# Kernel tuning notes

Hardware: AMD Instinct MI355X
Metric: run time of the kernel (lower is better)

The kernel has to match this reference:

```python
import jax, jax.numpy as jnp
import numpy as np

FEATURE_DIM = 512
NUM_HEADS = 8
HEAD_DIM = FEATURE_DIM // NUM_HEADS
B, L = 4, 2048


def setup_inputs() -> dict:
    key = jax.random.key(0)
    ks = jax.random.split(key, 10)
    s = 1.0 / np.sqrt(FEATURE_DIM)
    inp = {
        "ppg": jax.random.normal(ks[0], (B, FEATURE_DIM, L), dtype=jnp.float32),
        "ecg": jax.random.normal(ks[1], (B, FEATURE_DIM, L), dtype=jnp.float32),
        "Wq": jax.random.uniform(ks[2], (FEATURE_DIM, FEATURE_DIM), jnp.float32, -s, s),
        "bq": jnp.zeros((FEATURE_DIM,), jnp.float32),
        "Wk": jax.random.uniform(ks[3], (FEATURE_DIM, FEATURE_DIM), jnp.float32, -s, s),
        "bk": jnp.zeros((FEATURE_DIM,), jnp.float32),
        "Wv": jax.random.uniform(ks[4], (FEATURE_DIM, FEATURE_DIM), jnp.float32, -s, s),
        "bv": jnp.zeros((FEATURE_DIM,), jnp.float32),
        "Wo": jax.random.uniform(ks[5], (FEATURE_DIM, FEATURE_DIM), jnp.float32, -s, s),
        "bo": jnp.zeros((FEATURE_DIM,), jnp.float32),
    }
    return inp


def reference(ppg, ecg, Wq, bq, Wk, bk, Wv, bv, Wo, bo):
    # ppg/ecg: (B, C, L) -> (B, L, C)
    x = jnp.transpose(ppg, (0, 2, 1))
    y = jnp.transpose(ecg, (0, 2, 1))
    q = x @ Wq.T + bq  # (B, L, C)
    k = y @ Wk.T + bk
    v = y @ Wv.T + bv
    # split heads: (B, H, L, D)
    def split(t):
        return jnp.transpose(t.reshape(B, L, NUM_HEADS, HEAD_DIM), (0, 2, 1, 3))
    qh, kh, vh = split(q), split(k), split(v)
    scores = jnp.einsum('bhqd,bhkd->bhqk', qh, kh) / jnp.sqrt(jnp.float32(HEAD_DIM))
    probs = jax.nn.softmax(scores, axis=-1)  # dropout is identity in eval mode
    ctx = jnp.einsum('bhqk,bhkd->bhqd', probs, vh)
    ctx = jnp.transpose(ctx, (0, 2, 1, 3)).reshape(B, L, FEATURE_DIM)
    out = ctx @ Wo.T + bo + x  # residual with transposed ppg
    return jnp.transpose(out, (0, 2, 1))  # (B, C, L)
```

## Files before the change

### kernel.cpp

```cpp
#include <hip/hip_runtime.h>
#include <hip/hip_bf16.h>

static constexpr int Bc = 4;
static constexpr int Lc = 2048;
static constexpr int Cc = 512;
static constexpr int Hc = 8;
static constexpr int Dc = 64;

using short8  = __attribute__((ext_vector_type(8))) short;
using float4v = __attribute__((ext_vector_type(4))) float;

static __device__ __forceinline__ unsigned short f2bf(float f) {
    __hip_bfloat16 h = __float2bfloat16(f);
    return *reinterpret_cast<unsigned short*>(&h);
}
static __device__ __forceinline__ float bf2f(unsigned short u) {
    return __uint_as_float(((unsigned int)u) << 16);
}

__global__ __launch_bounds__(256) void prep_kernel(
    const float* __restrict__ ppg, const float* __restrict__ ecg,
    const float* __restrict__ Wq, const float* __restrict__ Wk,
    const float* __restrict__ Wv, const float* __restrict__ Wo,
    unsigned short* __restrict__ Xt_ppg, unsigned short* __restrict__ Xt_ecg,
    unsigned short* __restrict__ Wbf)
{
    __shared__ float Ts[64 * 69];
    const int task = blockIdx.x;
    const int tid  = threadIdx.x;

    if (task < 2048) {
        const int src = task >> 10;
        const int rem = task & 1023;
        const int b   = rem >> 8;
        const int c0  = ((rem >> 5) & 7) * 64;
        const int l0  = (rem & 31) * 64;
        const float* X = src ? ecg : ppg;
        unsigned short* Xt = src ? Xt_ecg : Xt_ppg;

        #pragma unroll
        for (int j = 0; j < 4; ++j) {
            int idx = tid + j * 256;
            int c = idx >> 4, l4 = idx & 15;
            float4 v = *(const float4*)(X + ((size_t)b * Cc + c0 + c) * Lc + l0 + l4 * 4);
            Ts[c * 69 + l4 * 4 + 0] = v.x;
            Ts[c * 69 + l4 * 4 + 1] = v.y;
            Ts[c * 69 + l4 * 4 + 2] = v.z;
            Ts[c * 69 + l4 * 4 + 3] = v.w;
        }
        __syncthreads();
        #pragma unroll
        for (int j = 0; j < 8; ++j) {
            int u = tid + j * 256;
            int l = u >> 5, p2 = u & 31;
            float a = Ts[(2 * p2) * 69 + l];
            float bb = Ts[(2 * p2 + 1) * 69 + l];
            ushort2 pk; pk.x = f2bf(a); pk.y = f2bf(bb);
            *(ushort2*)(Xt + ((size_t)b * Lc + l0 + l) * Cc + c0 + 2 * p2) = pk;
        }
    } else {
        const int wb   = task - 2048;
        const int widx = wb >> 7;
        const float* W = widx == 0 ? Wq : widx == 1 ? Wk : widx == 2 ? Wv : Wo;
        size_t off = (size_t)(wb & 127) * 2048 + (size_t)tid * 8;
        float4 v0 = *(const float4*)(W + off);
        float4 v1 = *(const float4*)(W + off + 4);
        unsigned short pk[8] = {f2bf(v0.x), f2bf(v0.y), f2bf(v0.z), f2bf(v0.w),
                                f2bf(v1.x), f2bf(v1.y), f2bf(v1.z), f2bf(v1.w)};
        *(short8*)(Wbf + (size_t)widx * Cc * Cc + off) = *(const short8*)pk;
    }
}

__global__ __launch_bounds__(256) void proj_kernel(
    const unsigned short* __restrict__ Xt_ppg,
    const unsigned short* __restrict__ Xt_ecg,
    const unsigned short* __restrict__ Wbf,
    const float* __restrict__ bq, const float* __restrict__ bk,
    const float* __restrict__ bv,
    unsigned short* __restrict__ Qw, unsigned short* __restrict__ Kw,
    unsigned short* __restrict__ Vtw)
{
    constexpr int LDW = 72;
    const int z = blockIdx.z, p = z >> 2, b = z & 3;
    const int l0 = blockIdx.x * 128, n0 = blockIdx.y * 128;
    const unsigned short* X = (p == 0) ? Xt_ppg : Xt_ecg;
    const unsigned short* W = Wbf + (size_t)p * Cc * Cc;
    const float* bias = (p == 0) ? bq : (p == 1) ? bk : bv;

    const int tid = threadIdx.x, wave = tid >> 6, lane = tid & 63;
    const int l16 = lane & 15, quad = lane >> 4;
    const int wr = wave >> 1, wc = wave & 1;

    __shared__ __align__(16) unsigned short At[128 * LDW];
    __shared__ __align__(16) unsigned short Bt[128 * LDW];

    float4v acc[4][4] = {};
    short8 areg[4], breg[4];

    const int srow = tid >> 3, sc8 = tid & 7;
    #pragma unroll
    for (int j = 0; j < 4; ++j) {
        areg[j] = *(const short8*)(X + ((size_t)b * Lc + l0 + srow + j * 32) * Cc + sc8 * 8);
        breg[j] = *(const short8*)(W + (size_t)(n0 + srow + j * 32) * Cc + sc8 * 8);
    }

    for (int c0 = 0; c0 < Cc; c0 += 64) {
        #pragma unroll
        for (int j = 0; j < 4; ++j) {
            *(short8*)&At[(srow + j * 32) * LDW + sc8 * 8] = areg[j];
            *(short8*)&Bt[(srow + j * 32) * LDW + sc8 * 8] = breg[j];
        }
        __syncthreads();

        if (c0 + 64 < Cc) {
            #pragma unroll
            for (int j = 0; j < 4; ++j) {
                areg[j] = *(const short8*)(X + ((size_t)b * Lc + l0 + srow + j * 32) * Cc
                                           + c0 + 64 + sc8 * 8);
                breg[j] = *(const short8*)(W + (size_t)(n0 + srow + j * 32) * Cc
                                           + c0 + 64 + sc8 * 8);
            }
        }

        const unsigned short* Am = (p < 2) ? At : Bt;
        const unsigned short* Bm = (p < 2) ? Bt : At;

        #pragma unroll
        for (int ks = 0; ks < 2; ++ks) {
            short8 bf[4];
            #pragma unroll
            for (int nt = 0; nt < 4; ++nt)
                bf[nt] = *(const short8*)&Bm[(wc * 64 + nt * 16 + l16) * LDW
                                             + ks * 32 + quad * 8];
            #pragma unroll
            for (int mt = 0; mt < 4; ++mt) {
                short8 af = *(const short8*)&Am[(wr * 64 + mt * 16 + l16) * LDW
                                                + ks * 32 + quad * 8];
                #pragma unroll
                for (int nt = 0; nt < 4; ++nt)
                    acc[mt][nt] = __builtin_amdgcn_mfma_f32_16x16x32_bf16(
                        af, bf[nt], acc[mt][nt], 0, 0, 0);
            }
        }
        __syncthreads();
    }

    if (p < 2) {
        const float sc = (p == 0) ? 0.18033688011112042f : 1.0f;
        unsigned short* dst = (p == 0) ? Qw : Kw;
        #pragma unroll
        for (int nt = 0; nt < 4; ++nt) {
            int n = n0 + wc * 64 + nt * 16 + l16;
            int h = n >> 6, d = n & 63;
            int bh = b * Hc + h;
            float bia = bias[n];
            #pragma unroll
            for (int mt = 0; mt < 4; ++mt) {
                #pragma unroll
                for (int r = 0; r < 4; ++r) {
                    int l = l0 + wr * 64 + mt * 16 + quad * 4 + r;
                    dst[((size_t)bh * Lc + l) * Dc + d] =
                        f2bf((acc[mt][nt][r] + bia) * sc);
                }
            }
        }
    } else {
        #pragma unroll
        for (int mt = 0; mt < 4; ++mt) {
            #pragma unroll
            for (int r = 0; r < 4; ++r) {
                int n = n0 + wr * 64 + mt * 16 + quad * 4 + r;
                int h = n >> 6, d = n & 63;
                int bh = b * Hc + h;
                float bia = bias[n];
                #pragma unroll
                for (int nt = 0; nt < 4; ++nt) {
                    int l = l0 + wc * 64 + nt * 16 + l16;
                    Vtw[((size_t)bh * Dc + d) * Lc + l] = f2bf(acc[mt][nt][r] + bia);
                }
            }
        }
    }
}

__global__ __launch_bounds__(256, 4) void attn_mfma_kernel(
    const unsigned short* __restrict__ Qg,
    const unsigned short* __restrict__ Kg,
    const unsigned short* __restrict__ Vtg,
    unsigned short* __restrict__ O0,
    unsigned short* __restrict__ O1,
    float* __restrict__ lpart)
{
    constexpr int LDW = 72;
    const int bh    = blockIdx.y;
    const int split = blockIdx.z;
    const int q0    = blockIdx.x * 128;
    const int tid   = threadIdx.x;
    const int wave  = tid >> 6;
    const int lane  = tid & 63;
    const int l16   = lane & 15;
    const int quad  = lane >> 4;

    __shared__ __align__(16) unsigned short Kt[64 * LDW];
    __shared__ __align__(16) unsigned short Vt[64 * LDW];
    __shared__ __align__(16) unsigned short PT[128 * LDW];

    const int srow = tid >> 3, sc8 = tid & 7;

    const unsigned short* Qb = Qg + ((size_t)bh * Lc + q0) * Dc;
    #pragma unroll
    for (int j = 0; j < 4; ++j)
        *(short8*)&PT[(srow + j * 32) * LDW + sc8 * 8] =
            *(const short8*)(Qb + (srow + j * 32) * Dc + sc8 * 8);
    __syncthreads();

    short8 qf[2][2];
    #pragma unroll
    for (int qt = 0; qt < 2; ++qt)
        #pragma unroll
        for (int ks = 0; ks < 2; ++ks)
            qf[qt][ks] = *(const short8*)&PT[(wave * 32 + qt * 16 + l16) * LDW
                                             + ks * 32 + quad * 8];

    float4v O[2][4] = {};
    float lsum[2] = {0.0f, 0.0f};

    const unsigned short* Kb0 = Kg + (size_t)bh * Lc * Dc;
    const unsigned short* Vb0 = Vtg + (size_t)bh * (Dc * Lc);
    const int kbase = split * (Lc / 2);

    short8 kreg[2], vreg[2];
    #pragma unroll
    for (int j = 0; j < 2; ++j) {
        kreg[j] = *(const short8*)(Kb0 + (size_t)(kbase + srow + j * 32) * Dc + sc8 * 8);
        vreg[j] = *(const short8*)(Vb0 + (size_t)(srow + j * 32) * Lc + kbase + sc8 * 8);
    }

    for (int kc = kbase; kc < kbase + Lc / 2; kc += 64) {
        #pragma unroll
        for (int j = 0; j < 2; ++j) {
            *(short8*)&Kt[(srow + j * 32) * LDW + sc8 * 8] = kreg[j];
            *(short8*)&Vt[(srow + j * 32) * LDW + sc8 * 8] = vreg[j];
        }
        __syncthreads();

        if (kc + 64 < kbase + Lc / 2) {
            #pragma unroll
            for (int j = 0; j < 2; ++j) {
                kreg[j] = *(const short8*)(Kb0 + (size_t)(kc + 64 + srow + j * 32) * Dc
                                           + sc8 * 8);
                vreg[j] = *(const short8*)(Vb0 + (size_t)(srow + j * 32) * Lc
                                           + kc + 64 + sc8 * 8);
            }
        }

        float4v S[4][2];
        #pragma unroll
        for (int kt = 0; kt < 4; ++kt)
            #pragma unroll
            for (int qt = 0; qt < 2; ++qt)
                S[kt][qt] = (float4v){0.f, 0.f, 0.f, 0.f};
        #pragma unroll
        for (int ks = 0; ks < 2; ++ks) {
            #pragma unroll
            for (int kt = 0; kt < 4; ++kt) {
                short8 af = *(const short8*)&Kt[(kt * 16 + l16) * LDW
                                                + ks * 32 + quad * 8];
                #pragma unroll
                for (int qt = 0; qt < 2; ++qt)
                    S[kt][qt] = __builtin_amdgcn_mfma_f32_16x16x32_bf16(
                        af, qf[qt][ks], S[kt][qt], 0, 0, 0);
            }
        }

        #pragma unroll
        for (int qt = 0; qt < 2; ++qt) {
            #pragma unroll
            for (int kt = 0; kt < 4; ++kt) {
                float p0 = __builtin_amdgcn_exp2f(S[kt][qt][0]);
                float p1 = __builtin_amdgcn_exp2f(S[kt][qt][1]);
                float p2 = __builtin_amdgcn_exp2f(S[kt][qt][2]);
                float p3 = __builtin_amdgcn_exp2f(S[kt][qt][3]);
                lsum[qt] += (p0 + p1) + (p2 + p3);
                ushort4 pk;
                pk.x = f2bf(p0); pk.y = f2bf(p1); pk.z = f2bf(p2); pk.w = f2bf(p3);
                *(ushort4*)&PT[(wave * 32 + qt * 16 + l16) * LDW
                               + kt * 16 + quad * 4] = pk;
            }
        }

        #pragma unroll
        for (int ks = 0; ks < 2; ++ks) {
            short8 pf[2];
            #pragma unroll
            for (int qt = 0; qt < 2; ++qt)
                pf[qt] = *(const short8*)&PT[(wave * 32 + qt * 16 + l16) * LDW
                                             + ks * 32 + quad * 8];
            #pragma unroll
            for (int dt = 0; dt < 4; ++dt) {
                short8 vf = *(const short8*)&Vt[(dt * 16 + l16) * LDW
                                                + ks * 32 + quad * 8];
                #pragma unroll
                for (int qt = 0; qt < 2; ++qt)
                    O[qt][dt] = __builtin_amdgcn_mfma_f32_16x16x32_bf16(
                        pf[qt], vf, O[qt][dt], 0, 0, 0);
            }
        }
        __syncthreads();
    }

    const int b = bh >> 3, h = bh & 7;
    unsigned short* Om = split ? O1 : O0;
    float* lp = lpart + (size_t)split * (Bc * Hc) * Lc + (size_t)bh * Lc;

    #pragma unroll
    for (int qt = 0; qt < 2; ++qt) {
        float t = lsum[qt];
        t += __shfl_xor(t, 16, 64);
        t += __shfl_xor(t, 32, 64);
        if (quad == 0)
            lp[q0 + wave * 32 + qt * 16 + l16] = t;
        #pragma unroll
        for (int dt = 0; dt < 4; ++dt) {
            #pragma unroll
            for (int r = 0; r < 4; ++r) {
                int q = q0 + wave * 32 + qt * 16 + quad * 4 + r;
                Om[((size_t)b * Lc + q) * Cc + h * Dc + dt * 16 + l16] =
                    f2bf(O[qt][dt][r]);
            }
        }
    }
}

__global__ __launch_bounds__(256) void outproj_kernel(
    const unsigned short* __restrict__ O0, const unsigned short* __restrict__ O1,
    const float* __restrict__ lpart,
    const unsigned short* __restrict__ Wo_bf,
    const float* __restrict__ bo, const float* __restrict__ ppg,
    float* __restrict__ out)
{
    constexpr int LDW = 72;
    const int b = blockIdx.z;
    const int l0 = blockIdx.x * 128, n0 = blockIdx.y * 128;
    const int tid = threadIdx.x, wave = tid >> 6, lane = tid & 63;
    const int l16 = lane & 15, quad = lane >> 4;
    const int wr = wave >> 1, wc = wave & 1;

    __shared__ __align__(16) unsigned short At[128 * LDW];
    __shared__ __align__(16) unsigned short Bt[128 * LDW];

    float4v acc[4][4] = {};
    const int srow = tid >> 3, sc8 = tid & 7;
    const size_t lplane = (size_t)(Bc * Hc) * Lc;

    for (int c0 = 0; c0 < Cc; c0 += 64) {
        const int h = c0 >> 6;
        const float* lp0 = lpart + (size_t)(b * Hc + h) * Lc;
        const float* lp1 = lp0 + lplane;

        #pragma unroll
        for (int j = 0; j < 4; ++j) {
            int row = srow + j * 32;
            *(short8*)&At[row * LDW + sc8 * 8] =
                *(const short8*)(Wo_bf + (size_t)(n0 + row) * Cc + c0 + sc8 * 8);
            int l = l0 + row;
            float inv = 1.0f / (lp0[l] + lp1[l]);
            size_t off = ((size_t)b * Lc + l) * Cc + c0 + sc8 * 8;
            short8 a8 = *(const short8*)(O0 + off);
            short8 b8 = *(const short8*)(O1 + off);
            unsigned short pk[8];
            #pragma unroll
            for (int e = 0; e < 8; ++e) {
                unsigned short ua = ((const unsigned short*)&a8)[e];
                unsigned short ub = ((const unsigned short*)&b8)[e];
                pk[e] = f2bf((bf2f(ua) + bf2f(ub)) * inv);
            }
            *(short8*)&Bt[row * LDW + sc8 * 8] = *(const short8*)pk;
        }
        __syncthreads();

        #pragma unroll
        for (int ks = 0; ks < 2; ++ks) {
            short8 bfr[4];
            #pragma unroll
            for (int nt = 0; nt < 4; ++nt)
                bfr[nt] = *(const short8*)&Bt[(wc * 64 + nt * 16 + l16) * LDW
                                              + ks * 32 + quad * 8];
            #pragma unroll
            for (int mt = 0; mt < 4; ++mt) {
                short8 af = *(const short8*)&At[(wr * 64 + mt * 16 + l16) * LDW
                                                + ks * 32 + quad * 8];
                #pragma unroll
                for (int nt = 0; nt < 4; ++nt)
                    acc[mt][nt] = __builtin_amdgcn_mfma_f32_16x16x32_bf16(
                        af, bfr[nt], acc[mt][nt], 0, 0, 0);
            }
        }
        __syncthreads();
    }

    #pragma unroll
    for (int mt = 0; mt < 4; ++mt) {
        #pragma unroll
        for (int r = 0; r < 4; ++r) {
            int n = n0 + wr * 64 + mt * 16 + quad * 4 + r;
            float bia = bo[n];
            #pragma unroll
            for (int nt = 0; nt < 4; ++nt) {
                int l = l0 + wc * 64 + nt * 16 + l16;
                size_t oidx = ((size_t)b * Cc + n) * Lc + l;
                out[oidx] = acc[mt][nt][r] + bia + ppg[oidx];
            }
        }
    }
}

extern "C" void kernel_launch(void* const* d_in, const int* in_sizes, int n_in,
                              void* d_out, int out_size, void* d_ws, size_t ws_size,
                              hipStream_t stream) {
    const float* ppg = (const float*)d_in[0];
    const float* ecg = (const float*)d_in[1];
    const float* Wq  = (const float*)d_in[2];
    const float* bq  = (const float*)d_in[3];
    const float* Wk  = (const float*)d_in[4];
    const float* bk  = (const float*)d_in[5];
    const float* Wv  = (const float*)d_in[6];
    const float* bv  = (const float*)d_in[7];
    const float* Wo  = (const float*)d_in[8];
    const float* bo  = (const float*)d_in[9];
    float* out = (float*)d_out;

    unsigned short* base   = (unsigned short*)d_ws;
    const size_t M = 1024 * 1024;
    unsigned short* Xt_ppg = base;
    unsigned short* Xt_ecg = base + 4 * M;
    unsigned short* Wbf    = base + 8 * M;
    unsigned short* Qw     = base + 9 * M;
    unsigned short* Kw     = base + 13 * M;
    unsigned short* Vtw    = base + 17 * M;
    float* lpart = (float*)(base + 21 * M);
    unsigned short* Opart0 = base;
    unsigned short* Opart1 = base + 4 * M;

    prep_kernel<<<2560, 256, 0, stream>>>(ppg, ecg, Wq, Wk, Wv, Wo,
                                          Xt_ppg, Xt_ecg, Wbf);

    dim3 g1(Lc / 128, Cc / 128, 3 * Bc);
    proj_kernel<<<g1, 256, 0, stream>>>(Xt_ppg, Xt_ecg, Wbf, bq, bk, bv,
                                        Qw, Kw, Vtw);

    dim3 g2(Lc / 128, Bc * Hc, 2);
    attn_mfma_kernel<<<g2, 256, 0, stream>>>(Qw, Kw, Vtw, Opart0, Opart1, lpart);

    dim3 g3(Lc / 128, Cc / 128, Bc);
    outproj_kernel<<<g3, 256, 0, stream>>>(Opart0, Opart1, lpart,
                                           Wbf + (size_t)3 * Cc * Cc,
                                           bo, ppg, out);
}
```

Before: 179.2 us.

## Rewrite attention core with 32x32 MFMA, register-resident P, async LDS double-buffering

Rewrites the attention kernel to use 32x32x16 bf16 MFMA tiles. The probabilities stay in registers via packed bf16 conversion and permlane32 swaps instead of round-tripping through shared memory. K/V tiles are loaded with global_load_lds into swizzled, double-buffered LDS, and blocks are remapped on a 1D grid to group same-head work onto the same XCD. This targets LDS traffic, bank conflicts and sync stalls, at the cost of relying on inline gfx950 asm and a precise lane layout that must match the MFMA operand format.

```diff
diff --git a/kernel.cpp b/kernel.cpp
--- a/kernel.cpp
+++ b/kernel.cpp
@@ -9,6 +9,7 @@
 
 using short8  = __attribute__((ext_vector_type(8))) short;
 using float4v = __attribute__((ext_vector_type(4))) float;
+using f32x16  = __attribute__((ext_vector_type(16))) float;
 
 static __device__ __forceinline__ unsigned short f2bf(float f) {
     __hip_bfloat16 h = __float2bfloat16(f);
@@ -16,6 +17,13 @@
 }
 static __device__ __forceinline__ float bf2f(unsigned short u) {
     return __uint_as_float(((unsigned int)u) << 16);
+}
+
+static __device__ __forceinline__ void gll16(const unsigned short* g, unsigned short* l) {
+    __builtin_amdgcn_global_load_lds(
+        (const __attribute__((address_space(1))) unsigned int*)g,
+        (__attribute__((address_space(3))) unsigned int*)l,
+        16, 0, 0);
 }
 
 __global__ __launch_bounds__(256) void prep_kernel(
@@ -191,143 +199,132 @@
     unsigned short* __restrict__ O1,
     float* __restrict__ lpart)
 {
-    constexpr int LDW = 72;
-    const int bh    = blockIdx.y;
-    const int split = blockIdx.z;
-    const int q0    = blockIdx.x * 128;
-    const int tid   = threadIdx.x;
-    const int wave  = tid >> 6;
-    const int lane  = tid & 63;
-    const int l16   = lane & 15;
-    const int quad  = lane >> 4;
-
-    __shared__ __align__(16) unsigned short Kt[64 * LDW];
-    __shared__ __align__(16) unsigned short Vt[64 * LDW];
-    __shared__ __align__(16) unsigned short PT[128 * LDW];
-
-    const int srow = tid >> 3, sc8 = tid & 7;
-
-    const unsigned short* Qb = Qg + ((size_t)bh * Lc + q0) * Dc;
+    const int bid = blockIdx.x;
+    const int r8  = bid & 7;
+    const int j   = bid >> 3;
+    const int g   = (j >> 4) * 8 + r8;
+    const int x   = j & 15;
+    const int bh    = g >> 1;
+    const int split = g & 1;
+    const int q0    = x * 128;
+
+    const int tid  = threadIdx.x;
+    const int wave = tid >> 6;
+    const int lane = tid & 63;
+    const int l32  = lane & 31;
+    const int hi   = lane >> 5;
+
+    __shared__ __align__(16) unsigned short Kt[2][64 * 64];
+    __shared__ __align__(16) unsigned short Vt[2][64 * 64];
+
+    const unsigned short* Kb = Kg  + (size_t)bh * Lc * Dc;
+    const unsigned short* Vb = Vtg + (size_t)bh * Dc * Lc;
+    const int kbase = split * (Lc / 2);
+
+    short8 qf[4];
+    const unsigned short* Qb =
+        Qg + ((size_t)bh * Lc + q0 + wave * 32 + l32) * Dc + hi * 8;
     #pragma unroll
-    for (int j = 0; j < 4; ++j)
-        *(short8*)&PT[(srow + j * 32) * LDW + sc8 * 8] =
-            *(const short8*)(Qb + (srow + j * 32) * Dc + sc8 * 8);
+    for (int st = 0; st < 4; ++st)
+        qf[st] = *(const short8*)(Qb + st * 16);
+
+    const int lrow8 = lane >> 3;
+    const int lslot = lane & 7;
+    auto STAGE = [&](int buf, int kc) {
+        #pragma unroll
+        for (int i = 0; i < 2; ++i) {
+            const int r = wave * 16 + i * 8 + lrow8;
+            const int sw = (lslot ^ (r & 7)) * 8;
+            gll16(Kb + (size_t)(kbase + kc + r) * Dc + sw,
+                  &Kt[buf][(wave * 16 + i * 8) * 64]);
+            gll16(Vb + (size_t)r * Lc + (kbase + kc) + sw,
+                  &Vt[buf][(wave * 16 + i * 8) * 64]);
+        }
+    };
+
+    STAGE(0, 0);
     __syncthreads();
 
-    short8 qf[2][2];
-    #pragma unroll
-    for (int qt = 0; qt < 2; ++qt)
-        #pragma unroll
-        for (int ks = 0; ks < 2; ++ks)
-            qf[qt][ks] = *(const short8*)&PT[(wave * 32 + qt * 16 + l16) * LDW
-                                             + ks * 32 + quad * 8];
-
-    float4v O[2][4] = {};
-    float lsum[2] = {0.0f, 0.0f};
-
-    const unsigned short* Kb0 = Kg + (size_t)bh * Lc * Dc;
-    const unsigned short* Vb0 = Vtg + (size_t)bh * (Dc * Lc);
-    const int kbase = split * (Lc / 2);
-
-    short8 kreg[2], vreg[2];
-    #pragma unroll
-    for (int j = 0; j < 2; ++j) {
-        kreg[j] = *(const short8*)(Kb0 + (size_t)(kbase + srow + j * 32) * Dc + sc8 * 8);
-        vreg[j] = *(const short8*)(Vb0 + (size_t)(srow + j * 32) * Lc + kbase + sc8 * 8);
-    }
-
-    for (int kc = kbase; kc < kbase + Lc / 2; kc += 64) {
-        #pragma unroll
-        for (int j = 0; j < 2; ++j) {
-            *(short8*)&Kt[(srow + j * 32) * LDW + sc8 * 8] = kreg[j];
-            *(short8*)&Vt[(srow + j * 32) * LDW + sc8 * 8] = vreg[j];
-        }
-        __syncthreads();
-
-        if (kc + 64 < kbase + Lc / 2) {
-            #pragma unroll
-            for (int j = 0; j < 2; ++j) {
-                kreg[j] = *(const short8*)(Kb0 + (size_t)(kc + 64 + srow + j * 32) * Dc
-                                           + sc8 * 8);
-                vreg[j] = *(const short8*)(Vb0 + (size_t)(srow + j * 32) * Lc
-                                           + kc + 64 + sc8 * 8);
-            }
-        }
-
-        float4v S[4][2];
-        #pragma unroll
-        for (int kt = 0; kt < 4; ++kt)
-            #pragma unroll
-            for (int qt = 0; qt < 2; ++qt)
-                S[kt][qt] = (float4v){0.f, 0.f, 0.f, 0.f};
-        #pragma unroll
-        for (int ks = 0; ks < 2; ++ks) {
-            #pragma unroll
-            for (int kt = 0; kt < 4; ++kt) {
-                short8 af = *(const short8*)&Kt[(kt * 16 + l16) * LDW
-                                                + ks * 32 + quad * 8];
-                #pragma unroll
-                for (int qt = 0; qt < 2; ++qt)
-                    S[kt][qt] = __builtin_amdgcn_mfma_f32_16x16x32_bf16(
-                        af, qf[qt][ks], S[kt][qt], 0, 0, 0);
-            }
-        }
-
-        #pragma unroll
-        for (int qt = 0; qt < 2; ++qt) {
-            #pragma unroll
-            for (int kt = 0; kt < 4; ++kt) {
-                float p0 = __builtin_amdgcn_exp2f(S[kt][qt][0]);
-                float p1 = __builtin_amdgcn_exp2f(S[kt][qt][1]);
-                float p2 = __builtin_amdgcn_exp2f(S[kt][qt][2]);
-                float p3 = __builtin_amdgcn_exp2f(S[kt][qt][3]);
-                lsum[qt] += (p0 + p1) + (p2 + p3);
-                ushort4 pk;
-                pk.x = f2bf(p0); pk.y = f2bf(p1); pk.z = f2bf(p2); pk.w = f2bf(p3);
-                *(ushort4*)&PT[(wave * 32 + qt * 16 + l16) * LDW
-                               + kt * 16 + quad * 4] = pk;
-            }
-        }
-
-        #pragma unroll
-        for (int ks = 0; ks < 2; ++ks) {
-            short8 pf[2];
-            #pragma unroll
-            for (int qt = 0; qt < 2; ++qt)
-                pf[qt] = *(const short8*)&PT[(wave * 32 + qt * 16 + l16) * LDW
-                                             + ks * 32 + quad * 8];
-            #pragma unroll
-            for (int dt = 0; dt < 4; ++dt) {
-                short8 vf = *(const short8*)&Vt[(dt * 16 + l16) * LDW
-                                                + ks * 32 + quad * 8];
-                #pragma unroll
-                for (int qt = 0; qt < 2; ++qt)
-                    O[qt][dt] = __builtin_amdgcn_mfma_f32_16x16x32_bf16(
-                        pf[qt], vf, O[qt][dt], 0, 0, 0);
-            }
-        }
-        __syncthreads();
-    }
-
+    f32x16 O[2] = {};
+    float lsum = 0.0f;
+
+    constexpr int NT = (Lc / 2) / 64;
+    for (int it = 0; it < NT; ++it) {
+        const int cur = it & 1;
+        if (it + 1 < NT) STAGE(cur ^ 1, (it + 1) * 64);
+
+        f32x16 S0, S1;
+        #pragma unroll
+        for (int e = 0; e < 16; ++e) { S0[e] = 0.0f; S1[e] = 0.0f; }
+        #pragma unroll
+        for (int st = 0; st < 4; ++st) {
+            const int slot = st * 2 + hi;
+            short8 k0 = *(const short8*)
+                &Kt[cur][l32 * 64 + ((slot ^ (l32 & 7)) * 8)];
+            short8 k1 = *(const short8*)
+                &Kt[cur][(32 + l32) * 64 + ((slot ^ (l32 & 7)) * 8)];
+            S0 = __builtin_amdgcn_mfma_f32_32x32x16_bf16(k0, qf[st], S0, 0, 0, 0);
+            S1 = __builtin_amdgcn_mfma_f32_32x32x16_bf16(k1, qf[st], S1, 0, 0, 0);
+        }
+
+        #pragma unroll
+        for (int kt = 0; kt < 2; ++kt) {
+            const f32x16& S = kt ? S1 : S0;
+            float p[16];
+            #pragma unroll
+            for (int e = 0; e < 16; ++e)
+                p[e] = __builtin_amdgcn_exp2f(S[e]);
+            #pragma unroll
+            for (int e = 0; e < 16; e += 4)
+                lsum += (p[e] + p[e + 1]) + (p[e + 2] + p[e + 3]);
+
+            unsigned int c[4][2];
+            #pragma unroll
+            for (int R = 0; R < 4; ++R) {
+                #pragma unroll
+                for (int w = 0; w < 2; ++w)
+                    asm("v_cvt_pk_bf16_f32 %0, %1, %2"
+                        : "=v"(c[R][w])
+                        : "v"(p[4 * R + 2 * w]), "v"(p[4 * R + 2 * w + 1]));
+            }
+
+            #pragma unroll
+            for (int ksl = 0; ksl < 2; ++ksl) {
+                unsigned int a0 = c[2 * ksl][0],     a1 = c[2 * ksl][1];
+                unsigned int a2 = c[2 * ksl + 1][0], a3 = c[2 * ksl + 1][1];
+                asm("v_permlane32_swap_b32 %0, %1" : "+v"(a0), "+v"(a2));
+                asm("v_permlane32_swap_b32 %0, %1" : "+v"(a1), "+v"(a3));
+                union { unsigned int w[4]; short8 s; } u;
+                u.w[0] = a0; u.w[1] = a1; u.w[2] = a2; u.w[3] = a3;
+
+                const int ksg = kt * 2 + ksl;
+                #pragma unroll
+                for (int dt = 0; dt < 2; ++dt) {
+                    const int row = dt * 32 + l32;
+                    short8 vf = *(const short8*)
+                        &Vt[cur][row * 64 + ((((ksg * 2) + hi) ^ (row & 7)) * 8)];
+                    O[dt] = __builtin_amdgcn_mfma_f32_32x32x16_bf16(
+                        u.s, vf, O[dt], 0, 0, 0);
+                }
+            }
+        }
+        if (it + 1 < NT) __syncthreads();
+    }
+
+    lsum += __shfl_xor(lsum, 32, 64);
     const int b = bh >> 3, h = bh & 7;
     unsigned short* Om = split ? O1 : O0;
     float* lp = lpart + (size_t)split * (Bc * Hc) * Lc + (size_t)bh * Lc;
+    if (hi == 0)
+        lp[q0 + wave * 32 + l32] = lsum;
 
     #pragma unroll
-    for (int qt = 0; qt < 2; ++qt) {
-        float t = lsum[qt];
-        t += __shfl_xor(t, 16, 64);
-        t += __shfl_xor(t, 32, 64);
-        if (quad == 0)
-            lp[q0 + wave * 32 + qt * 16 + l16] = t;
-        #pragma unroll
-        for (int dt = 0; dt < 4; ++dt) {
-            #pragma unroll
-            for (int r = 0; r < 4; ++r) {
-                int q = q0 + wave * 32 + qt * 16 + quad * 4 + r;
-                Om[((size_t)b * Lc + q) * Cc + h * Dc + dt * 16 + l16] =
-                    f2bf(O[qt][dt][r]);
-            }
+    for (int dt = 0; dt < 2; ++dt) {
+        #pragma unroll
+        for (int e = 0; e < 16; ++e) {
+            const int q = q0 + wave * 32 + (e & 3) + 8 * (e >> 2) + 4 * hi;
+            Om[((size_t)b * Lc + q) * Cc + h * Dc + dt * 32 + l32] =
+                f2bf(O[dt][e]);
         }
     }
 }
@@ -449,8 +446,7 @@
     proj_kernel<<<g1, 256, 0, stream>>>(Xt_ppg, Xt_ecg, Wbf, bq, bk, bv,
                                         Qw, Kw, Vtw);
 
-    dim3 g2(Lc / 128, Bc * Hc, 2);
-    attn_mfma_kernel<<<g2, 256, 0, stream>>>(Qw, Kw, Vtw, Opart0, Opart1, lpart);
+    attn_mfma_kernel<<<1024, 256, 0, stream>>>(Qw, Kw, Vtw, Opart0, Opart1, lpart);
 
     dim3 g3(Lc / 128, Cc / 128, Bc);
     outproj_kernel<<<g3, 256, 0, stream>>>(Opart0, Opart1, lpart,
```

After: 179.2 us, median of 2. About the same (+0.0%).
